# Kernel tuning notes

Measured on AMD Instinct MI355X. Metric: run time of the kernel, lower is better.

Reference implementation:

```python
import jax, jax.numpy as jnp
import numpy as np

N = 1536       # number of agents in the group
T = 20         # track length (only last step used)
H = 64         # hidden_size
E = 16         # embadding_size
M = 128        # PNMLP_hidden_size


def setup_inputs() -> dict:
    key = jax.random.key(0)
    ks = jax.random.split(key, 8)
    s = lambda fan_in: 1.0 / np.sqrt(fan_in)
    return {
        "hidden_state": jax.random.normal(ks[0], (N, H), dtype=jnp.float32),
        "group_track": jax.random.normal(ks[1], (N, T, 2), dtype=jnp.float32),
        "We": jax.random.uniform(ks[2], (2, E), jnp.float32, -s(2), s(2)),
        "be": jax.random.uniform(ks[3], (E,), jnp.float32, -s(2), s(2)),
        "W1": jax.random.uniform(ks[4], (E + H, M), jnp.float32, -s(E + H), s(E + H)),
        "b1": jax.random.uniform(ks[5], (M,), jnp.float32, -s(E + H), s(E + H)),
        "W2": jax.random.uniform(ks[6], (M, H), jnp.float32, -s(M), s(M)),
        "b2": jax.random.uniform(ks[7], (H,), jnp.float32, -s(M), s(M)),
    }


def reference(hidden_state, group_track, We, be, W1, b1, W2, b2):
    # end positions of every track: [N, 2]
    end = group_track[:, -1, :]
    # rel[i, j] = end[j] - end[i]  (neighbor j relative to center i): [N, N, 2]
    rel = end[None, :, :] - end[:, None, :]
    # linear embedding of relative end positions: [N, N, E]
    emb = rel @ We + be
    # concat hidden state (same for all centers) with embedding: [N, N, E+H]
    h = jnp.broadcast_to(hidden_state[None, :, :], (rel.shape[0], rel.shape[1], hidden_state.shape[1]))
    x = jnp.concatenate((h, emb), axis=-1)
    # MLP [E+H -> M -> H] with ReLU after each linear (batch_norm=False)
    x = jax.nn.relu(x @ W1 + b1)
    x = jax.nn.relu(x @ W2 + b2)
    # max-pool over neighbors j for each center i: [N, H]
    return jnp.max(x, axis=1)
```

## Files before the change

### kernel.cpp

```cpp
#include <hip/hip_runtime.h>
#include <hip/hip_fp16.h>


#define NN 1536
#define HH 64
#define EE 16
#define MM 128
#define TT 20
#define NI 3
#define JSPLIT 4
#define NIGRP (NN / NI)
#define NTILE (96 / JSPLIT)

typedef _Float16 half8 __attribute__((ext_vector_type(8)));
typedef float f32x4 __attribute__((ext_vector_type(4)));

__global__ __launch_bounds__(128) void precompute_kernel(
    const float* __restrict__ hidden, const float* __restrict__ gt,
    const float* __restrict__ We, const float* __restrict__ be,
    const float* __restrict__ W1, const float* __restrict__ b1,
    _Float16* __restrict__ Q, _Float16* __restrict__ P, float* __restrict__ out)
{
  const int j = blockIdx.x;
  const int m = threadIdx.x;
  const float* hrow = hidden + j * HH;
  float a = 0.f;
  #pragma unroll 8
  for (int h = 0; h < HH; ++h) a = fmaf(hrow[h], W1[h * MM + m], a);
  float ve0 = 0.f, ve1 = 0.f, cm = b1[m];
  #pragma unroll
  for (int e = 0; e < EE; ++e) {
    float w1e = W1[(HH + e) * MM + m];
    ve0 = fmaf(We[e], w1e, ve0);
    ve1 = fmaf(We[EE + e], w1e, ve1);
    cm  = fmaf(be[e], w1e, cm);
  }
  const float e0 = gt[j * (2 * TT) + 2 * (TT - 1)];
  const float e1 = gt[j * (2 * TT) + 2 * (TT - 1) + 1];
  const float p = fmaf(e0, ve0, e1 * ve1);
  P[j * MM + m] = (_Float16)p;
  Q[j * MM + m] = (_Float16)(a + p + cm);
  if (m < HH) out[j * HH + m] = 0.f;
}

__global__ __launch_bounds__(64, 2) void pairmlp_max_kernel(
    const _Float16* __restrict__ Q, const _Float16* __restrict__ P,
    const float* __restrict__ W2, const float* __restrict__ b2,
    float* __restrict__ out)
{
  const int lane = threadIdx.x;
  const int quad = lane >> 4;
  const int lcol = lane & 15;
  const int ig = blockIdx.x % NIGRP;
  const int js = blockIdx.x / NIGRP;
  const int i0 = ig * NI;

  half8 bfrag[4][4];
  float b2v[4];
  #pragma unroll
  for (int ct = 0; ct < 4; ++ct) {
    const int col = ct * 16 + lcol;
    b2v[ct] = b2[col];
    #pragma unroll
    for (int ks = 0; ks < 4; ++ks) {
      half8 b;
      #pragma unroll
      for (int jj = 0; jj < 8; ++jj)
        b[jj] = (_Float16)W2[(ks * 32 + quad * 8 + jj) * HH + col];
      bfrag[ct][ks] = b;
    }
  }

  half8 pv[NI][4];
  #pragma unroll
  for (int ii = 0; ii < NI; ++ii) {
    const _Float16* prow = P + (i0 + ii) * MM + quad * 8;
    #pragma unroll
    for (int ks = 0; ks < 4; ++ks)
      pv[ii][ks] = *(const half8*)(prow + ks * 32);
  }

  float rmax[NI][4];
  #pragma unroll
  for (int ii = 0; ii < NI; ++ii)
    #pragma unroll
    for (int ct = 0; ct < 4; ++ct) rmax[ii][ct] = 0.f;

  const int jt0 = js * NTILE;
  const _Float16* qbase = Q + lcol * MM + quad * 8;

  half8 qc[4], qn[4];
  #pragma unroll
  for (int ks = 0; ks < 4; ++ks)
    qc[ks] = *(const half8*)(qbase + (jt0 * 16) * MM + ks * 32);

  const half8 hz = 0;

  for (int t = 0; t < NTILE; ++t) {
    const int jl = (t + 1 < NTILE) ? (jt0 + t + 1) : jt0;
    #pragma unroll
    for (int ks = 0; ks < 4; ++ks)
      qn[ks] = *(const half8*)(qbase + (jl * 16) * MM + ks * 32);

    f32x4 acc[NI][4];
    #pragma unroll
    for (int ii = 0; ii < NI; ++ii)
      #pragma unroll
      for (int ct = 0; ct < 4; ++ct) acc[ii][ct] = f32x4{0.f, 0.f, 0.f, 0.f};

    #pragma unroll
    for (int ks = 0; ks < 4; ++ks) {
      #pragma unroll
      for (int ii = 0; ii < NI; ++ii) {
        half8 s = qc[ks] - pv[ii][ks];
        s = __builtin_elementwise_max(s, hz);
        #pragma unroll
        for (int ct = 0; ct < 4; ++ct)
          acc[ii][ct] = __builtin_amdgcn_mfma_f32_16x16x32_f16(s, bfrag[ct][ks], acc[ii][ct], 0, 0, 0);
      }
    }

    #pragma unroll
    for (int ii = 0; ii < NI; ++ii)
      #pragma unroll
      for (int ct = 0; ct < 4; ++ct) {
        const float m01 = fmaxf(acc[ii][ct][0], acc[ii][ct][1]);
        const float m23 = fmaxf(acc[ii][ct][2], acc[ii][ct][3]);
        rmax[ii][ct] = fmaxf(rmax[ii][ct], fmaxf(m01, m23) + b2v[ct]);
      }

    #pragma unroll
    for (int ks = 0; ks < 4; ++ks) qc[ks] = qn[ks];
  }

  #pragma unroll
  for (int ii = 0; ii < NI; ++ii)
    #pragma unroll
    for (int ct = 0; ct < 4; ++ct) {
      float v = rmax[ii][ct];
      v = fmaxf(v, __shfl_xor(v, 16, 64));
      v = fmaxf(v, __shfl_xor(v, 32, 64));
      if (quad == 0)
        atomicMax((unsigned*)(out + (i0 + ii) * HH + ct * 16 + lcol), __float_as_uint(v));
    }
}

extern "C" void kernel_launch(void* const* d_in, const int* in_sizes, int n_in,
                              void* d_out, int out_size, void* d_ws, size_t ws_size,
                              hipStream_t stream) {
  const float* hidden = (const float*)d_in[0];
  const float* gt     = (const float*)d_in[1];
  const float* We     = (const float*)d_in[2];
  const float* be     = (const float*)d_in[3];
  const float* W1     = (const float*)d_in[4];
  const float* b1     = (const float*)d_in[5];
  const float* W2     = (const float*)d_in[6];
  const float* b2     = (const float*)d_in[7];
  float* out = (float*)d_out;

  _Float16* Qh = (_Float16*)d_ws;
  _Float16* Ph = Qh + NN * MM;

  precompute_kernel<<<NN, 128, 0, stream>>>(hidden, gt, We, be, W1, b1, Qh, Ph, out);
  pairmlp_max_kernel<<<NIGRP * JSPLIT, 64, 0, stream>>>(Qh, Ph, W2, b2, out);
}
```

Before: 110.0 us.

## Pre-transpose W2 to fp16, split neighbors six ways, unroll tile loop

The precompute kernel now writes a transposed fp16 copy of W2, so the pair kernel can load its B fragments as vector loads instead of 128 strided scalar fp32 loads per thread. The neighbor split rises from 4 to 6 for more blocks, and the tile loop is manually unrolled by two with ping-pong Q buffers. The first MFMA of each tile now takes a zero accumulator, and the b2 bias plus ReLU move to after the final max reduction. Deferring the bias is valid because max commutes with adding a per-column constant, and the ReLU is then applied to the final result. The added risks are an extra workspace buffer, and 16 tiles per block requiring an even tile count for the two-way unroll.

```diff
diff --git a/kernel.cpp b/kernel.cpp
--- a/kernel.cpp
+++ b/kernel.cpp
@@ -8,7 +8,7 @@
 #define MM 128
 #define TT 20
 #define NI 3
-#define JSPLIT 4
+#define JSPLIT 6
 #define NIGRP (NN / NI)
 #define NTILE (96 / JSPLIT)
 
@@ -19,7 +19,9 @@
     const float* __restrict__ hidden, const float* __restrict__ gt,
     const float* __restrict__ We, const float* __restrict__ be,
     const float* __restrict__ W1, const float* __restrict__ b1,
-    _Float16* __restrict__ Q, _Float16* __restrict__ P, float* __restrict__ out)
+    const float* __restrict__ W2,
+    _Float16* __restrict__ Q, _Float16* __restrict__ P,
+    _Float16* __restrict__ W2T, float* __restrict__ out)
 {
   const int j = blockIdx.x;
   const int m = threadIdx.x;
@@ -40,12 +42,13 @@
   const float p = fmaf(e0, ve0, e1 * ve1);
   P[j * MM + m] = (_Float16)p;
   Q[j * MM + m] = (_Float16)(a + p + cm);
+  if (j < HH) W2T[j * MM + m] = (_Float16)W2[m * HH + j];
   if (m < HH) out[j * HH + m] = 0.f;
 }
 
 __global__ __launch_bounds__(64, 2) void pairmlp_max_kernel(
     const _Float16* __restrict__ Q, const _Float16* __restrict__ P,
-    const float* __restrict__ W2, const float* __restrict__ b2,
+    const _Float16* __restrict__ W2T, const float* __restrict__ b2,
     float* __restrict__ out)
 {
   const int lane = threadIdx.x;
@@ -56,19 +59,12 @@
   const int i0 = ig * NI;
 
   half8 bfrag[4][4];
-  float b2v[4];
   #pragma unroll
   for (int ct = 0; ct < 4; ++ct) {
-    const int col = ct * 16 + lcol;
-    b2v[ct] = b2[col];
+    const _Float16* wrow = W2T + (ct * 16 + lcol) * MM + quad * 8;
     #pragma unroll
-    for (int ks = 0; ks < 4; ++ks) {
-      half8 b;
-      #pragma unroll
-      for (int jj = 0; jj < 8; ++jj)
-        b[jj] = (_Float16)W2[(ks * 32 + quad * 8 + jj) * HH + col];
-      bfrag[ct][ks] = b;
-    }
+    for (int ks = 0; ks < 4; ++ks)
+      bfrag[ct][ks] = *(const half8*)(wrow + ks * 32);
   }
 
   half8 pv[NI][4];
@@ -84,54 +80,65 @@
   #pragma unroll
   for (int ii = 0; ii < NI; ++ii)
     #pragma unroll
-    for (int ct = 0; ct < 4; ++ct) rmax[ii][ct] = 0.f;
+    for (int ct = 0; ct < 4; ++ct) rmax[ii][ct] = -1e30f;
 
   const int jt0 = js * NTILE;
-  const _Float16* qbase = Q + lcol * MM + quad * 8;
-
-  half8 qc[4], qn[4];
-  #pragma unroll
-  for (int ks = 0; ks < 4; ++ks)
-    qc[ks] = *(const half8*)(qbase + (jt0 * 16) * MM + ks * 32);
+  const _Float16* qbase = Q + (jt0 * 16 + lcol) * MM + quad * 8;
 
   const half8 hz = 0;
+  const f32x4 zc = {0.f, 0.f, 0.f, 0.f};
 
-  for (int t = 0; t < NTILE; ++t) {
-    const int jl = (t + 1 < NTILE) ? (jt0 + t + 1) : jt0;
+  #define PROCESS_TILE(QT)                                                        \
+    do {                                                                          \
+      f32x4 acc[NI][4];                                                           \
+      _Pragma("unroll")                                                           \
+      for (int ii = 0; ii < NI; ++ii) {                                           \
+        half8 s = (QT)[0] - pv[ii][0];                                            \
+        s = __builtin_elementwise_max(s, hz);                                     \
+        _Pragma("unroll")                                                         \
+        for (int ct = 0; ct < 4; ++ct)                                            \
+          acc[ii][ct] = __builtin_amdgcn_mfma_f32_16x16x32_f16(s, bfrag[ct][0], zc, 0, 0, 0); \
+      }                                                                           \
+      _Pragma("unroll")                                                           \
+      for (int ks = 1; ks < 4; ++ks) {                                            \
+        _Pragma("unroll")                                                         \
+        for (int ii = 0; ii < NI; ++ii) {                                         \
+          half8 s = (QT)[ks] - pv[ii][ks];                                        \
+          s = __builtin_elementwise_max(s, hz);                                   \
+          _Pragma("unroll")                                                       \
+          for (int ct = 0; ct < 4; ++ct)                                          \
+            acc[ii][ct] = __builtin_amdgcn_mfma_f32_16x16x32_f16(s, bfrag[ct][ks], acc[ii][ct], 0, 0, 0); \
+        }                                                                         \
+      }                                                                           \
+      _Pragma("unroll")                                                           \
+      for (int ii = 0; ii < NI; ++ii)                                             \
+        _Pragma("unroll")                                                         \
+        for (int ct = 0; ct < 4; ++ct) {                                          \
+          const float m01 = fmaxf(acc[ii][ct][0], acc[ii][ct][1]);                \
+          const float m23 = fmaxf(acc[ii][ct][2], acc[ii][ct][3]);                \
+          rmax[ii][ct] = fmaxf(rmax[ii][ct], fmaxf(m01, m23));                    \
+        }                                                                         \
+    } while (0)
+
+  half8 qa[4], qb[4];
+  #pragma unroll
+  for (int ks = 0; ks < 4; ++ks) qa[ks] = *(const half8*)(qbase + ks * 32);
+
+  for (int t = 0; t < NTILE; t += 2) {
+    const _Float16* q1 = qbase + (t + 1) * 16 * MM;
     #pragma unroll
-    for (int ks = 0; ks < 4; ++ks)
-      qn[ks] = *(const half8*)(qbase + (jl * 16) * MM + ks * 32);
+    for (int ks = 0; ks < 4; ++ks) qb[ks] = *(const half8*)(q1 + ks * 32);
 
-    f32x4 acc[NI][4];
+    PROCESS_TILE(qa);
+
+    const int t2 = (t + 2 < NTILE) ? (t + 2) : 0;
+    const _Float16* q2 = qbase + t2 * 16 * MM;
     #pragma unroll
-    for (int ii = 0; ii < NI; ++ii)
-      #pragma unroll
-      for (int ct = 0; ct < 4; ++ct) acc[ii][ct] = f32x4{0.f, 0.f, 0.f, 0.f};
+    for (int ks = 0; ks < 4; ++ks) qa[ks] = *(const half8*)(q2 + ks * 32);
 
-    #pragma unroll
-    for (int ks = 0; ks < 4; ++ks) {
-      #pragma unroll
-      for (int ii = 0; ii < NI; ++ii) {
-        half8 s = qc[ks] - pv[ii][ks];
-        s = __builtin_elementwise_max(s, hz);
-        #pragma unroll
-        for (int ct = 0; ct < 4; ++ct)
-          acc[ii][ct] = __builtin_amdgcn_mfma_f32_16x16x32_f16(s, bfrag[ct][ks], acc[ii][ct], 0, 0, 0);
-      }
-    }
-
-    #pragma unroll
-    for (int ii = 0; ii < NI; ++ii)
-      #pragma unroll
-      for (int ct = 0; ct < 4; ++ct) {
-        const float m01 = fmaxf(acc[ii][ct][0], acc[ii][ct][1]);
-        const float m23 = fmaxf(acc[ii][ct][2], acc[ii][ct][3]);
-        rmax[ii][ct] = fmaxf(rmax[ii][ct], fmaxf(m01, m23) + b2v[ct]);
-      }
-
-    #pragma unroll
-    for (int ks = 0; ks < 4; ++ks) qc[ks] = qn[ks];
+    PROCESS_TILE(qb);
   }
+  #undef PROCESS_TILE
 
   #pragma unroll
   for (int ii = 0; ii < NI; ++ii)
@@ -140,6 +147,7 @@
       float v = rmax[ii][ct];
       v = fmaxf(v, __shfl_xor(v, 16, 64));
       v = fmaxf(v, __shfl_xor(v, 32, 64));
+      v = fmaxf(v + b2[ct * 16 + lcol], 0.f);
       if (quad == 0)
         atomicMax((unsigned*)(out + (i0 + ii) * HH + ct * 16 + lcol), __float_as_uint(v));
     }
@@ -158,9 +166,10 @@
   const float* b2     = (const float*)d_in[7];
   float* out = (float*)d_out;
 
-  _Float16* Qh = (_Float16*)d_ws;
-  _Float16* Ph = Qh + NN * MM;
+  _Float16* Qh  = (_Float16*)d_ws;
+  _Float16* Ph  = Qh + NN * MM;
+  _Float16* W2T = Ph + NN * MM;
 
-  precompute_kernel<<<NN, 128, 0, stream>>>(hidden, gt, We, be, W1, b1, Qh, Ph, out);
-  pairmlp_max_kernel<<<NIGRP * JSPLIT, 64, 0, stream>>>(Qh, Ph, W2, b2, out);
+  precompute_kernel<<<NN, 128, 0, stream>>>(hidden, gt, We, be, W1, b1, W2, Qh, Ph, W2T, out);
+  pairmlp_max_kernel<<<NIGRP * JSPLIT, 64, 0, stream>>>(Qh, Ph, W2T, b2, out);
 }
```

New measurement: 116.2 us. 5.7% more time.

## Pre-transpose W2 to fp16, shrink per-block rows, defer bias/ReLU to final reduction

Applied to the files above, without the earlier changes.

The precompute kernel now writes an fp16 transposed copy of W2, so each pair-MLP block loads its B fragments with vector loads instead of 8 strided scalar float loads per fragment. The pair kernel processes 2 centers per block instead of 3 and splits the neighbour range into 8 parts instead of 4. It drops the Q double-buffering, raises launch_bounds occupancy to 3, seeds the first MFMA with a zero accumulator, and applies b2 and ReLU once after the max reduction rather than on every tile. The aim is lower register pressure and setup cost and more blocks in flight, at the price of more atomics and more redundant W2 fragment loads across blocks.

```diff
diff --git a/kernel.cpp b/kernel.cpp
--- a/kernel.cpp
+++ b/kernel.cpp
@@ -7,19 +7,24 @@
 #define EE 16
 #define MM 128
 #define TT 20
-#define NI 3
-#define JSPLIT 4
+#define NI 2
+#define JSPLIT 8
 #define NIGRP (NN / NI)
 #define NTILE (96 / JSPLIT)
 
 typedef _Float16 half8 __attribute__((ext_vector_type(8)));
+typedef _Float16 half2v __attribute__((ext_vector_type(2)));
 typedef float f32x4 __attribute__((ext_vector_type(4)));
+
+union H8 { half8 v; half2v h2[4]; };
 
 __global__ __launch_bounds__(128) void precompute_kernel(
     const float* __restrict__ hidden, const float* __restrict__ gt,
     const float* __restrict__ We, const float* __restrict__ be,
     const float* __restrict__ W1, const float* __restrict__ b1,
-    _Float16* __restrict__ Q, _Float16* __restrict__ P, float* __restrict__ out)
+    const float* __restrict__ W2,
+    _Float16* __restrict__ Q, _Float16* __restrict__ P,
+    _Float16* __restrict__ W2T, float* __restrict__ out)
 {
   const int j = blockIdx.x;
   const int m = threadIdx.x;
@@ -40,12 +45,13 @@
   const float p = fmaf(e0, ve0, e1 * ve1);
   P[j * MM + m] = (_Float16)p;
   Q[j * MM + m] = (_Float16)(a + p + cm);
+  if (j < HH) W2T[j * MM + m] = (_Float16)W2[m * HH + j];
   if (m < HH) out[j * HH + m] = 0.f;
 }
 
-__global__ __launch_bounds__(64, 2) void pairmlp_max_kernel(
+__global__ __launch_bounds__(64, 3) void pairmlp_max_kernel(
     const _Float16* __restrict__ Q, const _Float16* __restrict__ P,
-    const float* __restrict__ W2, const float* __restrict__ b2,
+    const _Float16* __restrict__ W2T, const float* __restrict__ b2,
     float* __restrict__ out)
 {
   const int lane = threadIdx.x;
@@ -56,67 +62,63 @@
   const int i0 = ig * NI;
 
   half8 bfrag[4][4];
-  float b2v[4];
   #pragma unroll
   for (int ct = 0; ct < 4; ++ct) {
-    const int col = ct * 16 + lcol;
-    b2v[ct] = b2[col];
+    const _Float16* wrow = W2T + (ct * 16 + lcol) * MM + quad * 8;
     #pragma unroll
-    for (int ks = 0; ks < 4; ++ks) {
-      half8 b;
-      #pragma unroll
-      for (int jj = 0; jj < 8; ++jj)
-        b[jj] = (_Float16)W2[(ks * 32 + quad * 8 + jj) * HH + col];
-      bfrag[ct][ks] = b;
-    }
+    for (int ks = 0; ks < 4; ++ks)
+      bfrag[ct][ks] = *(const half8*)(wrow + ks * 32);
   }
 
-  half8 pv[NI][4];
+  H8 pv[NI][4];
   #pragma unroll
   for (int ii = 0; ii < NI; ++ii) {
     const _Float16* prow = P + (i0 + ii) * MM + quad * 8;
     #pragma unroll
     for (int ks = 0; ks < 4; ++ks)
-      pv[ii][ks] = *(const half8*)(prow + ks * 32);
+      pv[ii][ks].v = *(const half8*)(prow + ks * 32);
   }
 
   float rmax[NI][4];
   #pragma unroll
   for (int ii = 0; ii < NI; ++ii)
     #pragma unroll
-    for (int ct = 0; ct < 4; ++ct) rmax[ii][ct] = 0.f;
+    for (int ct = 0; ct < 4; ++ct) rmax[ii][ct] = -1e30f;
 
   const int jt0 = js * NTILE;
-  const _Float16* qbase = Q + lcol * MM + quad * 8;
+  const _Float16* qptr = Q + (jt0 * 16 + lcol) * MM + quad * 8;
 
-  half8 qc[4], qn[4];
-  #pragma unroll
-  for (int ks = 0; ks < 4; ++ks)
-    qc[ks] = *(const half8*)(qbase + (jt0 * 16) * MM + ks * 32);
+  const half2v hz2 = {(_Float16)0.f, (_Float16)0.f};
+  const f32x4 zc = {0.f, 0.f, 0.f, 0.f};
 
-  const half8 hz = 0;
-
+  #pragma unroll 1
   for (int t = 0; t < NTILE; ++t) {
-    const int jl = (t + 1 < NTILE) ? (jt0 + t + 1) : jt0;
+    H8 q[4];
     #pragma unroll
     for (int ks = 0; ks < 4; ++ks)
-      qn[ks] = *(const half8*)(qbase + (jl * 16) * MM + ks * 32);
+      q[ks].v = *(const half8*)(qptr + ks * 32);
+    qptr += 16 * MM;
 
     f32x4 acc[NI][4];
-    #pragma unroll
-    for (int ii = 0; ii < NI; ++ii)
-      #pragma unroll
-      for (int ct = 0; ct < 4; ++ct) acc[ii][ct] = f32x4{0.f, 0.f, 0.f, 0.f};
-
     #pragma unroll
     for (int ks = 0; ks < 4; ++ks) {
       #pragma unroll
       for (int ii = 0; ii < NI; ++ii) {
-        half8 s = qc[ks] - pv[ii][ks];
-        s = __builtin_elementwise_max(s, hz);
+        H8 s;
         #pragma unroll
-        for (int ct = 0; ct < 4; ++ct)
-          acc[ii][ct] = __builtin_amdgcn_mfma_f32_16x16x32_f16(s, bfrag[ct][ks], acc[ii][ct], 0, 0, 0);
+        for (int r = 0; r < 4; ++r) {
+          half2v d = q[ks].h2[r] - pv[ii][ks].h2[r];
+          s.h2[r] = __builtin_elementwise_max(d, hz2);
+        }
+        if (ks == 0) {
+          #pragma unroll
+          for (int ct = 0; ct < 4; ++ct)
+            acc[ii][ct] = __builtin_amdgcn_mfma_f32_16x16x32_f16(s.v, bfrag[ct][0], zc, 0, 0, 0);
+        } else {
+          #pragma unroll
+          for (int ct = 0; ct < 4; ++ct)
+            acc[ii][ct] = __builtin_amdgcn_mfma_f32_16x16x32_f16(s.v, bfrag[ct][ks], acc[ii][ct], 0, 0, 0);
+        }
       }
     }
 
@@ -126,11 +128,8 @@
       for (int ct = 0; ct < 4; ++ct) {
         const float m01 = fmaxf(acc[ii][ct][0], acc[ii][ct][1]);
         const float m23 = fmaxf(acc[ii][ct][2], acc[ii][ct][3]);
-        rmax[ii][ct] = fmaxf(rmax[ii][ct], fmaxf(m01, m23) + b2v[ct]);
+        rmax[ii][ct] = fmaxf(rmax[ii][ct], fmaxf(m01, m23));
       }
-
-    #pragma unroll
-    for (int ks = 0; ks < 4; ++ks) qc[ks] = qn[ks];
   }
 
   #pragma unroll
@@ -140,6 +139,7 @@
       float v = rmax[ii][ct];
       v = fmaxf(v, __shfl_xor(v, 16, 64));
       v = fmaxf(v, __shfl_xor(v, 32, 64));
+      v = fmaxf(v + b2[ct * 16 + lcol], 0.f);
       if (quad == 0)
         atomicMax((unsigned*)(out + (i0 + ii) * HH + ct * 16 + lcol), __float_as_uint(v));
     }
@@ -158,9 +158,10 @@
   const float* b2     = (const float*)d_in[7];
   float* out = (float*)d_out;
 
-  _Float16* Qh = (_Float16*)d_ws;
-  _Float16* Ph = Qh + NN * MM;
+  _Float16* Qh  = (_Float16*)d_ws;
+  _Float16* Ph  = Qh + NN * MM;
+  _Float16* W2T = Ph + NN * MM;
 
-  precompute_kernel<<<NN, 128, 0, stream>>>(hidden, gt, We, be, W1, b1, Qh, Ph, out);
-  pairmlp_max_kernel<<<NIGRP * JSPLIT, 64, 0, stream>>>(Qh, Ph, W2, b2, out);
+  precompute_kernel<<<NN, 128, 0, stream>>>(hidden, gt, We, be, W1, b1, W2, Qh, Ph, W2T, out);
+  pairmlp_max_kernel<<<NIGRP * JSPLIT, 64, 0, stream>>>(Qh, Ph, W2T, b2, out);
 }
```

Result: slower. 126.3 us (+14.8%).
